# Kernel tuning notes

Hardware: AMD Instinct MI355X
Metric: run time of the kernel (lower is better)

The kernel has to match this reference:

```python
import jax, jax.numpy as jnp
import numpy as np

N_NODES = 50000
N_EDGES = 800000
IN_F = 256
OUT_F = 128
ALPHA = 0.2  # LeakyReLU negative slope


def setup_inputs() -> dict:
    key = jax.random.key(0)
    k_h, k_row, k_col, k_W, k_a = jax.random.split(key, 5)
    h = jax.random.normal(k_h, (N_NODES, IN_F), dtype=jnp.float32)
    row = jax.random.randint(k_row, (N_EDGES,), 0, N_NODES)
    # Guarantee every node appears as a destination so unique(dst) == arange(N)
    col = jnp.concatenate([
        jnp.arange(N_NODES),
        jax.random.randint(k_col, (N_EDGES - N_NODES,), 0, N_NODES),
    ])
    adj = jnp.stack([row, col]).astype(jnp.int64)
    # Xavier-uniform-ish params (gain 1.414)
    lim_W = 1.414 * np.sqrt(6.0 / (IN_F + OUT_F))
    W = jax.random.uniform(k_W, (IN_F, OUT_F), minval=-lim_W, maxval=lim_W, dtype=jnp.float32)
    lim_a = 1.414 * np.sqrt(6.0 / (2 * OUT_F + 1))
    a = jax.random.uniform(k_a, (2 * OUT_F, 1), minval=-lim_a, maxval=lim_a, dtype=jnp.float32)
    return {"h": h, "adj": adj, "W": W, "a": a}


def reference(h, adj, W, a):
    N = h.shape[0]
    self_loops = jnp.arange(N)  # == unique(adj[1]) by input construction
    row = jnp.concatenate([adj[0], self_loops])  # [E_total]
    col = jnp.concatenate([adj[1], self_loops])  # [E_total]

    Wh = h @ W                                    # [N, OUT_F]
    s_src = (Wh @ a[:OUT_F]).squeeze(-1)          # [N] (Wh1)
    s_dst = (Wh @ a[OUT_F:]).squeeze(-1)          # [N] (Wh2)

    e = jax.nn.leaky_relu(s_dst[col] + s_src[row], negative_slope=ALPHA)  # [E_total]

    # segment softmax over destination nodes
    e_max = jax.ops.segment_max(e, col, num_segments=N)
    ex = jnp.exp(e - e_max[col])
    denom = jax.ops.segment_sum(ex, col, num_segments=N)
    att = ex / denom[col]                         # [E_total]

    h_prime = jax.ops.segment_sum(Wh[row] * att[:, None], col, num_segments=N)  # [N, OUT_F]
    return jax.nn.elu(h_prime)  # concat=True
```

## Files before the change

kernel.cpp:

```cpp
#include <hip/hip_runtime.h>
#include <math.h>

#define N_NODES 50000
#define N_EDGES 800000
#define E_TOTAL (N_NODES + N_EDGES)
#define IN_F 256
#define OUT_F 128
#define ALPHA 0.2f

#define GEMM_WAVES ((N_NODES + 31) / 32)
#define GEMM_BLOCKS ((GEMM_WAVES + 3) / 4)

typedef short bf16x8 __attribute__((ext_vector_type(8)));
typedef float f32x4  __attribute__((ext_vector_type(4)));

static __device__ __forceinline__ unsigned short f2bf(float f) {
    unsigned int u = __float_as_uint(f);
    u += 0x7FFFu + ((u >> 16) & 1u);
    return (unsigned short)(u >> 16);
}
static __device__ __forceinline__ float bf2f(unsigned int u16) {
    return __uint_as_float(u16 << 16);
}

__global__ __launch_bounds__(256) void k_init(int* head) {
    int i = blockIdx.x * blockDim.x + threadIdx.x;
    if (i < N_NODES) head[i] = -1;
}

__global__ __launch_bounds__(256) void k_prep_wa(const float* __restrict__ W,
                                                 const float* __restrict__ a,
                                                 float* __restrict__ Wa) {
    int k = threadIdx.x;
    const float4* wr  = (const float4*)(W + (size_t)k * OUT_F);
    const float4* av1 = (const float4*)a;
    const float4* av2 = (const float4*)(a + OUT_F);
    float s1 = 0.0f, s2 = 0.0f;
#pragma unroll 8
    for (int i = 0; i < OUT_F / 4; ++i) {
        float4 w = wr[i], x = av1[i], y = av2[i];
        s1 = fmaf(w.x, x.x, fmaf(w.y, x.y, fmaf(w.z, x.z, fmaf(w.w, x.w, s1))));
        s2 = fmaf(w.x, y.x, fmaf(w.y, y.y, fmaf(w.z, y.z, fmaf(w.w, y.w, s2))));
    }
    Wa[k] = s1;
    Wa[IN_F + k] = s2;
}

__global__ __launch_bounds__(256) void k_prep_wt(const float* __restrict__ W,
                                                 unsigned short* __restrict__ WbT) {
    int n = blockIdx.x;
    int k = threadIdx.x;
    WbT[(size_t)n * IN_F + k] = f2bf(W[(size_t)k * OUT_F + n]);
}

__global__ __launch_bounds__(256) void k_gemm(const float* __restrict__ h,
                                              const unsigned short* __restrict__ WbT,
                                              const float* __restrict__ Wa,
                                              unsigned short* __restrict__ Whb,
                                              float* __restrict__ s_src,
                                              float* __restrict__ s_dst) {
    const int wid  = (blockIdx.x * blockDim.x + threadIdx.x) >> 6;
    const int lane = threadIdx.x & 63;
    if (wid >= GEMM_WAVES) return;
    const int m = lane & 15, grp = lane >> 4;
    const int row0 = wid * 32;

    f32x4 acc[2][8];
#pragma unroll
    for (int rt = 0; rt < 2; ++rt)
#pragma unroll
        for (int nt = 0; nt < 8; ++nt) acc[rt][nt] = (f32x4){0.f, 0.f, 0.f, 0.f};
    float sp1[2] = {0.f, 0.f}, sp2[2] = {0.f, 0.f};

    for (int kt = 0; kt < 8; ++kt) {
        const int k0 = kt * 32;
        bf16x8 hfrag[2];
#pragma unroll
        for (int rt = 0; rt < 2; ++rt) {
            int r = row0 + rt * 16 + m;
            if (r >= N_NODES) r = N_NODES - 1;
            const float4* hp = (const float4*)(h + (size_t)r * IN_F + k0 + grp * 8);
            float4 x0 = hp[0], x1 = hp[1];
            const float4* wap1 = (const float4*)(Wa + k0 + grp * 8);
            const float4* wap2 = (const float4*)(Wa + IN_F + k0 + grp * 8);
            float4 a0 = wap1[0], a1 = wap1[1];
            float4 b0 = wap2[0], b1 = wap2[1];
            sp1[rt] = fmaf(x0.x, a0.x, fmaf(x0.y, a0.y, fmaf(x0.z, a0.z, fmaf(x0.w, a0.w, sp1[rt]))));
            sp1[rt] = fmaf(x1.x, a1.x, fmaf(x1.y, a1.y, fmaf(x1.z, a1.z, fmaf(x1.w, a1.w, sp1[rt]))));
            sp2[rt] = fmaf(x0.x, b0.x, fmaf(x0.y, b0.y, fmaf(x0.z, b0.z, fmaf(x0.w, b0.w, sp2[rt]))));
            sp2[rt] = fmaf(x1.x, b1.x, fmaf(x1.y, b1.y, fmaf(x1.z, b1.z, fmaf(x1.w, b1.w, sp2[rt]))));
            bf16x8 hf;
            hf[0] = (short)f2bf(x0.x); hf[1] = (short)f2bf(x0.y);
            hf[2] = (short)f2bf(x0.z); hf[3] = (short)f2bf(x0.w);
            hf[4] = (short)f2bf(x1.x); hf[5] = (short)f2bf(x1.y);
            hf[6] = (short)f2bf(x1.z); hf[7] = (short)f2bf(x1.w);
            hfrag[rt] = hf;
        }
#pragma unroll
        for (int nt = 0; nt < 8; ++nt) {
            bf16x8 wf = *(const bf16x8*)(WbT + (size_t)(nt * 16 + m) * IN_F + k0 + grp * 8);
            acc[0][nt] = __builtin_amdgcn_mfma_f32_16x16x32_bf16(wf, hfrag[0], acc[0][nt], 0, 0, 0);
            acc[1][nt] = __builtin_amdgcn_mfma_f32_16x16x32_bf16(wf, hfrag[1], acc[1][nt], 0, 0, 0);
        }
    }

#pragma unroll
    for (int rt = 0; rt < 2; ++rt) {
        const int row = row0 + rt * 16 + m;
        const bool valid = (row < N_NODES);
        float t1 = sp1[rt], t2 = sp2[rt];
        t1 += __shfl_xor(t1, 16); t1 += __shfl_xor(t1, 32);
        t2 += __shfl_xor(t2, 16); t2 += __shfl_xor(t2, 32);
        if (valid && grp == 0) { s_src[row] = t1; s_dst[row] = t2; }
        if (valid) {
            unsigned short* orow = Whb + (size_t)row * OUT_F;
#pragma unroll
            for (int nt = 0; nt < 8; ++nt) {
                f32x4 v = acc[rt][nt];
                ushort4 pk;
                pk.x = f2bf(v[0]); pk.y = f2bf(v[1]);
                pk.z = f2bf(v[2]); pk.w = f2bf(v[3]);
                *(ushort4*)(orow + nt * 16 + grp * 4) = pk;
            }
        }
    }
}

__global__ __launch_bounds__(256) void k_link(const int* __restrict__ adj,
                                              int* __restrict__ head,
                                              int2* __restrict__ list) {
    int e = blockIdx.x * blockDim.x + threadIdx.x;
    if (e >= N_EDGES) return;
    int src = adj[e];
    int col = adj[N_EDGES + e];
    int old = atomicExch(&head[col], e);
    list[e] = make_int2(src, old);
}

__global__ __launch_bounds__(256) void k_gather(const unsigned short* __restrict__ Whb,
                                                const int* __restrict__ head,
                                                const int2* __restrict__ list,
                                                const float* __restrict__ s_src,
                                                const float* __restrict__ s_dst,
                                                float* __restrict__ out) {
    int wid  = (blockIdx.x * blockDim.x + threadIdx.x) >> 6;
    int tl   = threadIdx.x & 63;
    int half = tl >> 5;
    int l    = tl & 31;
    int node = wid * 2 + half;
    if (node >= N_NODES) return;

    float sd = s_dst[node];

    float s0 = sd + s_src[node];
    float lr0 = (s0 > 0.0f) ? s0 : ALPHA * s0;
    float x0 = __expf(lr0);
    uint2 w0 = *((const uint2*)(Whb + (size_t)node * OUT_F) + l);
    float4 acc;
    acc.x = x0 * bf2f(w0.x & 0xFFFFu);
    acc.y = x0 * bf2f(w0.x >> 16);
    acc.z = x0 * bf2f(w0.y & 0xFFFFu);
    acc.w = x0 * bf2f(w0.y >> 16);
    float dsum = x0;

    int e = head[node];
    while (e >= 0) {
        int2 rec = list[e];
        e = rec.y;
        float ss = s_src[rec.x];
        uint2 wv = *((const uint2*)(Whb + (size_t)rec.x * OUT_F) + l);
        float s = sd + ss;
        float lr = (s > 0.0f) ? s : ALPHA * s;
        float x = __expf(lr);
        acc.x = fmaf(x, bf2f(wv.x & 0xFFFFu), acc.x);
        acc.y = fmaf(x, bf2f(wv.x >> 16), acc.y);
        acc.z = fmaf(x, bf2f(wv.y & 0xFFFFu), acc.z);
        acc.w = fmaf(x, bf2f(wv.y >> 16), acc.w);
        dsum += x;
    }

    float inv = 1.0f / dsum;
    float4 v;
    v.x = acc.x * inv; v.y = acc.y * inv;
    v.z = acc.z * inv; v.w = acc.w * inv;
    v.x = (v.x > 0.0f) ? v.x : expm1f(v.x);
    v.y = (v.y > 0.0f) ? v.y : expm1f(v.y);
    v.z = (v.z > 0.0f) ? v.z : expm1f(v.z);
    v.w = (v.w > 0.0f) ? v.w : expm1f(v.w);
    *((float4*)(out + (size_t)node * OUT_F) + l) = v;
}

extern "C" void kernel_launch(void* const* d_in, const int* in_sizes, int n_in,
                              void* d_out, int out_size, void* d_ws, size_t ws_size,
                              hipStream_t stream) {
    const float* h   = (const float*)d_in[0];
    const int*   adj = (const int*)d_in[1];
    const float* W   = (const float*)d_in[2];
    const float* a   = (const float*)d_in[3];
    float* out = (float*)d_out;

    char* ws = (char*)d_ws;
    const size_t SZ_WHB = (size_t)N_NODES * OUT_F * 2;
    const size_t SZ_N   = 200704;
    unsigned short* Whb = (unsigned short*)(ws);
    float* s_src   = (float*)(ws + SZ_WHB);
    float* s_dst   = (float*)(ws + SZ_WHB + SZ_N);
    int*   head    = (int*)  (ws + SZ_WHB + 2 * SZ_N);
    float* Wa      = (float*)(ws + SZ_WHB + 3 * SZ_N);
    unsigned short* WbT = (unsigned short*)(ws + SZ_WHB + 3 * SZ_N + 2048);
    int2*  list    = (int2*) (ws + SZ_WHB + 3 * SZ_N + 2048 + 65536);

    (void)in_sizes; (void)n_in; (void)out_size; (void)ws_size;

    const int B = 256;
    k_init   <<<(N_NODES + B - 1) / B, B, 0, stream>>>(head);
    k_prep_wa<<<1, 256, 0, stream>>>(W, a, Wa);
    k_prep_wt<<<OUT_F, 256, 0, stream>>>(W, WbT);
    k_gemm   <<<GEMM_BLOCKS, 256, 0, stream>>>(h, WbT, Wa, Whb, s_src, s_dst);
    k_link   <<<(N_EDGES + B - 1) / B, B, 0, stream>>>(adj, head, list);
    k_gather <<<((N_NODES + 1) / 2 * 64 + B - 1) / B, B, 0, stream>>>(Whb, head, list,
                                                                      s_src, s_dst, out);
}
```

Baseline: 222.1 us.

## Split linked-list gather into walk+packed CSR gather and fuse prep/link kernels

The old per-node pointer-chasing gather is split into three steps. Per-node degree counts are taken during linking, offsets are assigned with an atomic, a one-thread-per-node walk writes packed (src, exp-score) pairs, and a wave-per-node gather then reads those pairs with 8-way unrolled independent loads. The aim is to take the serial dependent-load chain out of the bandwidth-heavy feature gather and to get more memory requests in flight. It also fuses the init and weight-prep kernels into one launch and runs edge linking inside the GEMM launch to cut launch count. In exchange it adds an extra pass that writes and reads roughly 7 MB of packed pairs, plus two small extra kernels.

```diff
diff --git a/kernel.cpp b/kernel.cpp
--- a/kernel.cpp
+++ b/kernel.cpp
@@ -10,6 +10,8 @@
 
 #define GEMM_WAVES ((N_NODES + 31) / 32)
 #define GEMM_BLOCKS ((GEMM_WAVES + 3) / 4)
+#define LINK_BLOCKS ((N_EDGES + 255) / 256)
+#define NODE_BLOCKS ((N_NODES + 255) / 256)
 
 typedef short bf16x8 __attribute__((ext_vector_type(8)));
 typedef float f32x4  __attribute__((ext_vector_type(4)));
@@ -23,43 +25,59 @@
     return __uint_as_float(u16 << 16);
 }
 
-__global__ __launch_bounds__(256) void k_init(int* head) {
-    int i = blockIdx.x * blockDim.x + threadIdx.x;
-    if (i < N_NODES) head[i] = -1;
-}
-
-__global__ __launch_bounds__(256) void k_prep_wa(const float* __restrict__ W,
-                                                 const float* __restrict__ a,
-                                                 float* __restrict__ Wa) {
-    int k = threadIdx.x;
-    const float4* wr  = (const float4*)(W + (size_t)k * OUT_F);
-    const float4* av1 = (const float4*)a;
-    const float4* av2 = (const float4*)(a + OUT_F);
-    float s1 = 0.0f, s2 = 0.0f;
+__global__ __launch_bounds__(256) void k_prep(const float* __restrict__ W,
+                                              const float* __restrict__ a,
+                                              int* __restrict__ head,
+                                              int* __restrict__ cnt,
+                                              int* __restrict__ total,
+                                              float* __restrict__ Wa,
+                                              unsigned short* __restrict__ WbT) {
+    const int b = blockIdx.x, t = threadIdx.x;
+    if (b < NODE_BLOCKS) {
+        int i = b * 256 + t;
+        if (i < N_NODES) { head[i] = -1; cnt[i] = 1; }
+    } else if (b == NODE_BLOCKS) {
+        if (t == 0) *total = 0;
+        const int k = t;
+        const float4* wr  = (const float4*)(W + (size_t)k * OUT_F);
+        const float4* av1 = (const float4*)a;
+        const float4* av2 = (const float4*)(a + OUT_F);
+        float s1 = 0.0f, s2 = 0.0f;
 #pragma unroll 8
-    for (int i = 0; i < OUT_F / 4; ++i) {
-        float4 w = wr[i], x = av1[i], y = av2[i];
-        s1 = fmaf(w.x, x.x, fmaf(w.y, x.y, fmaf(w.z, x.z, fmaf(w.w, x.w, s1))));
-        s2 = fmaf(w.x, y.x, fmaf(w.y, y.y, fmaf(w.z, y.z, fmaf(w.w, y.w, s2))));
-    }
-    Wa[k] = s1;
-    Wa[IN_F + k] = s2;
-}
-
-__global__ __launch_bounds__(256) void k_prep_wt(const float* __restrict__ W,
-                                                 unsigned short* __restrict__ WbT) {
-    int n = blockIdx.x;
-    int k = threadIdx.x;
-    WbT[(size_t)n * IN_F + k] = f2bf(W[(size_t)k * OUT_F + n]);
-}
-
-__global__ __launch_bounds__(256) void k_gemm(const float* __restrict__ h,
-                                              const unsigned short* __restrict__ WbT,
-                                              const float* __restrict__ Wa,
-                                              unsigned short* __restrict__ Whb,
-                                              float* __restrict__ s_src,
-                                              float* __restrict__ s_dst) {
-    const int wid  = (blockIdx.x * blockDim.x + threadIdx.x) >> 6;
+        for (int i = 0; i < OUT_F / 4; ++i) {
+            float4 w = wr[i], x = av1[i], y = av2[i];
+            s1 = fmaf(w.x, x.x, fmaf(w.y, x.y, fmaf(w.z, x.z, fmaf(w.w, x.w, s1))));
+            s2 = fmaf(w.x, y.x, fmaf(w.y, y.y, fmaf(w.z, y.z, fmaf(w.w, y.w, s2))));
+        }
+        Wa[k] = s1;
+        Wa[IN_F + k] = s2;
+    } else {
+        const int n = b - (NODE_BLOCKS + 1);
+        WbT[(size_t)n * IN_F + t] = f2bf(W[(size_t)t * OUT_F + n]);
+    }
+}
+
+__global__ __launch_bounds__(256) void k_gemm_link(const float* __restrict__ h,
+                                                   const unsigned short* __restrict__ WbT,
+                                                   const float* __restrict__ Wa,
+                                                   const int* __restrict__ adj,
+                                                   unsigned short* __restrict__ Whb,
+                                                   float* __restrict__ s_src,
+                                                   float* __restrict__ s_dst,
+                                                   int* __restrict__ head,
+                                                   int* __restrict__ cnt,
+                                                   int2* __restrict__ list) {
+    if (blockIdx.x >= GEMM_BLOCKS) {
+        int e = (blockIdx.x - GEMM_BLOCKS) * 256 + threadIdx.x;
+        if (e >= N_EDGES) return;
+        int src = adj[e];
+        int col = adj[N_EDGES + e];
+        int old = atomicExch(&head[col], e);
+        list[e] = make_int2(src, old);
+        atomicAdd(&cnt[col], 1);
+        return;
+    }
+    const int wid  = blockIdx.x * 4 + (threadIdx.x >> 6);
     const int lane = threadIdx.x & 63;
     if (wid >= GEMM_WAVES) return;
     const int m = lane & 15, grp = lane >> 4;
@@ -126,41 +144,30 @@
     }
 }
 
-__global__ __launch_bounds__(256) void k_link(const int* __restrict__ adj,
-                                              int* __restrict__ head,
-                                              int2* __restrict__ list) {
-    int e = blockIdx.x * blockDim.x + threadIdx.x;
-    if (e >= N_EDGES) return;
-    int src = adj[e];
-    int col = adj[N_EDGES + e];
-    int old = atomicExch(&head[col], e);
-    list[e] = make_int2(src, old);
-}
-
-__global__ __launch_bounds__(256) void k_gather(const unsigned short* __restrict__ Whb,
-                                                const int* __restrict__ head,
-                                                const int2* __restrict__ list,
-                                                const float* __restrict__ s_src,
-                                                const float* __restrict__ s_dst,
-                                                float* __restrict__ out) {
-    int wid  = (blockIdx.x * blockDim.x + threadIdx.x) >> 6;
-    int tl   = threadIdx.x & 63;
-    int half = tl >> 5;
-    int l    = tl & 31;
-    int node = wid * 2 + half;
+__global__ __launch_bounds__(256) void k_offsets(const int* __restrict__ cnt,
+                                                 int* __restrict__ start,
+                                                 int* __restrict__ total) {
+    int i = blockIdx.x * blockDim.x + threadIdx.x;
+    if (i >= N_NODES) return;
+    start[i] = atomicAdd(total, cnt[i]);
+}
+
+__global__ __launch_bounds__(256) void k_walk(const int* __restrict__ head,
+                                              const int2* __restrict__ list,
+                                              const float* __restrict__ s_src,
+                                              const float* __restrict__ s_dst,
+                                              const int* __restrict__ start,
+                                              int2* __restrict__ pack,
+                                              float* __restrict__ denom) {
+    int node = blockIdx.x * blockDim.x + threadIdx.x;
     if (node >= N_NODES) return;
-
     float sd = s_dst[node];
+    int p = start[node];
 
     float s0 = sd + s_src[node];
     float lr0 = (s0 > 0.0f) ? s0 : ALPHA * s0;
     float x0 = __expf(lr0);
-    uint2 w0 = *((const uint2*)(Whb + (size_t)node * OUT_F) + l);
-    float4 acc;
-    acc.x = x0 * bf2f(w0.x & 0xFFFFu);
-    acc.y = x0 * bf2f(w0.x >> 16);
-    acc.z = x0 * bf2f(w0.y & 0xFFFFu);
-    acc.w = x0 * bf2f(w0.y >> 16);
+    pack[p++] = make_int2(node, __float_as_int(x0));
     float dsum = x0;
 
     int e = head[node];
@@ -168,26 +175,73 @@
         int2 rec = list[e];
         e = rec.y;
         float ss = s_src[rec.x];
-        uint2 wv = *((const uint2*)(Whb + (size_t)rec.x * OUT_F) + l);
         float s = sd + ss;
         float lr = (s > 0.0f) ? s : ALPHA * s;
         float x = __expf(lr);
-        acc.x = fmaf(x, bf2f(wv.x & 0xFFFFu), acc.x);
-        acc.y = fmaf(x, bf2f(wv.x >> 16), acc.y);
-        acc.z = fmaf(x, bf2f(wv.y & 0xFFFFu), acc.z);
-        acc.w = fmaf(x, bf2f(wv.y >> 16), acc.w);
+        pack[p++] = make_int2(rec.x, __float_as_int(x));
         dsum += x;
     }
-
-    float inv = 1.0f / dsum;
-    float4 v;
-    v.x = acc.x * inv; v.y = acc.y * inv;
-    v.z = acc.z * inv; v.w = acc.w * inv;
-    v.x = (v.x > 0.0f) ? v.x : expm1f(v.x);
-    v.y = (v.y > 0.0f) ? v.y : expm1f(v.y);
-    v.z = (v.z > 0.0f) ? v.z : expm1f(v.z);
-    v.w = (v.w > 0.0f) ? v.w : expm1f(v.w);
-    *((float4*)(out + (size_t)node * OUT_F) + l) = v;
+    denom[node] = dsum;
+}
+
+__global__ __launch_bounds__(256) void k_gather(const unsigned short* __restrict__ Whb,
+                                                const int* __restrict__ start,
+                                                const int* __restrict__ cnt,
+                                                const int2* __restrict__ pack,
+                                                const float* __restrict__ denom,
+                                                float* __restrict__ out) {
+    int node = (blockIdx.x * blockDim.x + threadIdx.x) >> 6;
+    int lane = threadIdx.x & 63;
+    if (node >= N_NODES) return;
+    int s0 = start[node];
+    int n  = cnt[node];
+    const uint* __restrict__ Wv = (const uint*)Whb;
+
+    float ax = 0.0f, ay = 0.0f;
+    int j = 0;
+    for (; j + 8 <= n; j += 8) {
+        int2 p0 = pack[s0 + j + 0];
+        int2 p1 = pack[s0 + j + 1];
+        int2 p2 = pack[s0 + j + 2];
+        int2 p3 = pack[s0 + j + 3];
+        int2 p4 = pack[s0 + j + 4];
+        int2 p5 = pack[s0 + j + 5];
+        int2 p6 = pack[s0 + j + 6];
+        int2 p7 = pack[s0 + j + 7];
+        uint w0 = Wv[(size_t)p0.x * (OUT_F / 2) + lane];
+        uint w1 = Wv[(size_t)p1.x * (OUT_F / 2) + lane];
+        uint w2 = Wv[(size_t)p2.x * (OUT_F / 2) + lane];
+        uint w3 = Wv[(size_t)p3.x * (OUT_F / 2) + lane];
+        uint w4 = Wv[(size_t)p4.x * (OUT_F / 2) + lane];
+        uint w5 = Wv[(size_t)p5.x * (OUT_F / 2) + lane];
+        uint w6 = Wv[(size_t)p6.x * (OUT_F / 2) + lane];
+        uint w7 = Wv[(size_t)p7.x * (OUT_F / 2) + lane];
+        float x0 = __int_as_float(p0.y), x1 = __int_as_float(p1.y);
+        float x2 = __int_as_float(p2.y), x3 = __int_as_float(p3.y);
+        float x4 = __int_as_float(p4.y), x5 = __int_as_float(p5.y);
+        float x6 = __int_as_float(p6.y), x7 = __int_as_float(p7.y);
+        ax = fmaf(x0, bf2f(w0 & 0xFFFFu), ax); ay = fmaf(x0, bf2f(w0 >> 16), ay);
+        ax = fmaf(x1, bf2f(w1 & 0xFFFFu), ax); ay = fmaf(x1, bf2f(w1 >> 16), ay);
+        ax = fmaf(x2, bf2f(w2 & 0xFFFFu), ax); ay = fmaf(x2, bf2f(w2 >> 16), ay);
+        ax = fmaf(x3, bf2f(w3 & 0xFFFFu), ax); ay = fmaf(x3, bf2f(w3 >> 16), ay);
+        ax = fmaf(x4, bf2f(w4 & 0xFFFFu), ax); ay = fmaf(x4, bf2f(w4 >> 16), ay);
+        ax = fmaf(x5, bf2f(w5 & 0xFFFFu), ax); ay = fmaf(x5, bf2f(w5 >> 16), ay);
+        ax = fmaf(x6, bf2f(w6 & 0xFFFFu), ax); ay = fmaf(x6, bf2f(w6 >> 16), ay);
+        ax = fmaf(x7, bf2f(w7 & 0xFFFFu), ax); ay = fmaf(x7, bf2f(w7 >> 16), ay);
+    }
+    for (; j < n; ++j) {
+        int2 p = pack[s0 + j];
+        uint w = Wv[(size_t)p.x * (OUT_F / 2) + lane];
+        float x = __int_as_float(p.y);
+        ax = fmaf(x, bf2f(w & 0xFFFFu), ax);
+        ay = fmaf(x, bf2f(w >> 16), ay);
+    }
+    float inv = 1.0f / denom[node];
+    float vx = ax * inv;
+    float vy = ay * inv;
+    vx = (vx > 0.0f) ? vx : expm1f(vx);
+    vy = (vy > 0.0f) ? vy : expm1f(vy);
+    ((float2*)(out + (size_t)node * OUT_F))[lane] = make_float2(vx, vy);
 }
 
 extern "C" void kernel_launch(void* const* d_in, const int* in_sizes, int n_in,
@@ -202,22 +256,26 @@
     char* ws = (char*)d_ws;
     const size_t SZ_WHB = (size_t)N_NODES * OUT_F * 2;
     const size_t SZ_N   = 200704;
+    const size_t SZ_E8  = (size_t)N_EDGES * 8;
     unsigned short* Whb = (unsigned short*)(ws);
     float* s_src   = (float*)(ws + SZ_WHB);
     float* s_dst   = (float*)(ws + SZ_WHB + SZ_N);
     int*   head    = (int*)  (ws + SZ_WHB + 2 * SZ_N);
-    float* Wa      = (float*)(ws + SZ_WHB + 3 * SZ_N);
-    unsigned short* WbT = (unsigned short*)(ws + SZ_WHB + 3 * SZ_N + 2048);
-    int2*  list    = (int2*) (ws + SZ_WHB + 3 * SZ_N + 2048 + 65536);
+    int*   cnt     = (int*)  (ws + SZ_WHB + 3 * SZ_N);
+    int*   start   = (int*)  (ws + SZ_WHB + 4 * SZ_N);
+    float* denom   = (float*)(ws + SZ_WHB + 5 * SZ_N);
+    int*   total   = (int*)  (ws + SZ_WHB + 6 * SZ_N);
+    float* Wa      = (float*)(ws + SZ_WHB + 6 * SZ_N + 256);
+    unsigned short* WbT = (unsigned short*)(ws + SZ_WHB + 6 * SZ_N + 256 + 2048);
+    int2*  list    = (int2*) (ws + SZ_WHB + 6 * SZ_N + 256 + 2048 + 65536);
+    int2*  pack    = (int2*) (ws + SZ_WHB + 6 * SZ_N + 256 + 2048 + 65536 + SZ_E8);
 
     (void)in_sizes; (void)n_in; (void)out_size; (void)ws_size;
 
-    const int B = 256;
-    k_init   <<<(N_NODES + B - 1) / B, B, 0, stream>>>(head);
-    k_prep_wa<<<1, 256, 0, stream>>>(W, a, Wa);
-    k_prep_wt<<<OUT_F, 256, 0, stream>>>(W, WbT);
-    k_gemm   <<<GEMM_BLOCKS, 256, 0, stream>>>(h, WbT, Wa, Whb, s_src, s_dst);
-    k_link   <<<(N_EDGES + B - 1) / B, B, 0, stream>>>(adj, head, list);
-    k_gather <<<((N_NODES + 1) / 2 * 64 + B - 1) / B, B, 0, stream>>>(Whb, head, list,
-                                                                      s_src, s_dst, out);
-}
+    k_prep     <<<NODE_BLOCKS + 1 + OUT_F, 256, 0, stream>>>(W, a, head, cnt, total, Wa, WbT);
+    k_gemm_link<<<GEMM_BLOCKS + LINK_BLOCKS, 256, 0, stream>>>(h, WbT, Wa, adj, Whb,
+                                                               s_src, s_dst, head, cnt, list);
+    k_offsets  <<<NODE_BLOCKS, 256, 0, stream>>>(cnt, start, total);
+    k_walk     <<<NODE_BLOCKS, 256, 0, stream>>>(head, list, s_src, s_dst, start, pack, denom);
+    k_gather   <<<(N_NODES * 64 + 255) / 256, 256, 0, stream>>>(Whb, start, cnt, pack, denom, out);
+}
```

Result: slower. 235.9 us (+6.2%).
